# Performance work log

Hardware: AMD Instinct MI355X
Metric: run time of the kernel (lower is better)

Reference implementation:

```python
import jax, jax.numpy as jnp
import numpy as np
from math import sqrt

B, IN_C, OUT_C, H, W, WDIM, K = 16, 512, 512, 64, 64, 512, 3
EPS = 1e-8
LRELU_SLOPE = 0.2


def setup_inputs() -> dict:
    key = jax.random.key(0)
    ks = jax.random.split(key, 5)
    return {
        "x": jax.random.normal(ks[0], (B, IN_C, H, W), dtype=jnp.float32),
        "w": jax.random.normal(ks[1], (B, WDIM), dtype=jnp.float32),
        "noise": jax.random.normal(ks[2], (B, 1, H, W), dtype=jnp.float32),
        "linear_w": jax.random.normal(ks[3], (IN_C, WDIM), dtype=jnp.float32),
        "linear_b": jnp.ones((IN_C,), dtype=jnp.float32),
        "conv_w": jax.random.normal(ks[4], (OUT_C, IN_C, K, K), dtype=jnp.float32),
        "scale_noise": jnp.zeros((OUT_C,), dtype=jnp.float32),
        "bias": jnp.zeros((OUT_C,), dtype=jnp.float32),
    }


def reference(x, w, noise, linear_w, linear_b, conv_w, scale_noise, bias):
    # EqualizerStraights: equalized-lr linear, scale = 1/sqrt(w_dim)
    s = w @ (linear_w * (1.0 / sqrt(WDIM))).T + linear_b  # [b, in_c]
    # Weight_Demod: equalized conv weight, scale = 1/sqrt(in_c*k*k)
    base_w = conv_w * (1.0 / sqrt(IN_C * K * K))  # [out, in, k, k]
    weights = base_w[None] * s[:, None, :, None, None]  # [b, out, in, k, k]
    sigma_inv = jax.lax.rsqrt(
        jnp.sum(weights * weights, axis=(2, 3, 4), keepdims=True) + EPS)
    weights = weights * sigma_inv

    def conv1(xi, wi):  # xi [in,h,w], wi [out,in,k,k]
        return jax.lax.conv_general_dilated(
            xi[None], wi, window_strides=(1, 1), padding="SAME",
            dimension_numbers=("NCHW", "OIHW", "NCHW"))[0]

    y = jax.vmap(conv1)(x, weights)  # [b, out, h, w]
    y = y + scale_noise[None, :, None, None] * noise
    return jax.nn.leaky_relu(y + bias[None, :, None, None], negative_slope=LRELU_SLOPE)
```

## Files before the change

### kernel.cpp

```cpp
#include <hip/hip_runtime.h>
#include <hip/hip_bf16.h>
#include <stdint.h>

typedef __bf16 bf16_t;
typedef __bf16 bf16x8 __attribute__((ext_vector_type(8)));
typedef short short8 __attribute__((ext_vector_type(8)));
typedef float f32x4 __attribute__((ext_vector_type(4)));

#define RS512  0.044194173824159216f
#define RS4608 0.014731391274719739f

__global__ void k_style(const float* __restrict__ w, const float* __restrict__ lw,
                        const float* __restrict__ lb, float* __restrict__ s) {
  int b = blockIdx.y;
  int c = blockIdx.x * 256 + threadIdx.x;
  const float4* wr = (const float4*)(w + b * 512);
  const float4* lr = (const float4*)(lw + (size_t)c * 512);
  float acc = 0.f;
#pragma unroll 4
  for (int d = 0; d < 128; ++d) {
    float4 a = wr[d], q = lr[d];
    acc += a.x * q.x + a.y * q.y + a.z * q.z + a.w * q.w;
  }
  s[b * 512 + c] = acc * RS512 + lb[c];
}

__global__ void k_wprep(const float* __restrict__ cw, float* __restrict__ wsq,
                        bf16_t* __restrict__ bwf) {
  int idx = blockIdx.x * 256 + threadIdx.x;
  int o = idx >> 9, i = idx & 511;
  float v[9];
  float ss = 0.f;
#pragma unroll
  for (int t = 0; t < 9; ++t) {
    float x = cw[(size_t)idx * 9 + t] * RS4608;
    v[t] = x;
    ss += x * x;
  }
  wsq[idx] = ss;
  int lane = (o & 15) | (((i >> 3) & 3) << 4);
  int base_blk = (i >> 5) * 32 + (o >> 4);
#pragma unroll
  for (int t = 0; t < 9; ++t) {
    size_t e = ((size_t)(t * 512 + base_blk) << 9) + lane * 8 + (i & 7);
    bwf[e] = (bf16_t)v[t];
  }
}

__global__ void k_sigma(const float* __restrict__ s, const float* __restrict__ wsq,
                        float* __restrict__ sinv) {
  __shared__ float s2[512];
  int b = blockIdx.y;
  int o = blockIdx.x * 256 + threadIdx.x;
  for (int i = threadIdx.x; i < 512; i += 256) {
    float v = s[b * 512 + i];
    s2[i] = v * v;
  }
  __syncthreads();
  const float4* qr = (const float4*)(wsq + (size_t)o * 512);
  float acc = 0.f;
#pragma unroll 4
  for (int d = 0; d < 128; ++d) {
    float4 q = qr[d];
    acc += q.x * s2[4 * d] + q.y * s2[4 * d + 1] + q.z * s2[4 * d + 2] + q.w * s2[4 * d + 3];
  }
  sinv[b * 512 + o] = rsqrtf(acc + 1e-8f);
}

__global__ void k_xt(const float* __restrict__ x, const float* __restrict__ s,
                     bf16_t* __restrict__ xt) {
  int ic = blockIdx.x, h = blockIdx.y, b = blockIdx.z;
  __shared__ __align__(16) bf16_t tile[8192];
  int t = threadIdx.x;
  int wcol = t & 63;
  int g = t >> 6;
#pragma unroll
  for (int blk = 0; blk < 4; ++blk) {
    int grp = blk * 4 + g;
    bf16x8 vec;
#pragma unroll
    for (int k = 0; k < 8; ++k) {
      int i = ic * 128 + grp * 8 + k;
      float v = x[(((size_t)b * 512 + i) * 64 + h) * 64 + wcol] * s[b * 512 + i];
      vec[k] = (bf16_t)v;
    }
    int chunk = grp ^ (wcol & 15);
    *(bf16x8*)((char*)tile + wcol * 256 + chunk * 16) = vec;
  }
  __syncthreads();
#pragma unroll
  for (int j = 0; j < 4; ++j) {
    int flat = j * 256 + t;
    int wo = flat >> 4, ig8 = flat & 15;
    int chunk = ig8 ^ (wo & 15);
    bf16x8 v = *(bf16x8*)((char*)tile + wo * 256 + chunk * 16);
    int c32 = (ig8 >> 2);
    int slot = (ig8 & 3) ^ ((wo >> 1) & 3);
    *(bf16x8*)(xt + (((size_t)b * 64 + h) * 64 + wo) * 512 + ic * 128 + c32 * 32 + slot * 8) = v;
  }
}

#define AS1 __attribute__((address_space(1)))
#define AS3 __attribute__((address_space(3)))

__device__ __forceinline__ void gl16(const void* g, void* l) {
  __builtin_amdgcn_global_load_lds((const AS1 void*)g, (AS3 void*)l, 16, 0, 0);
}

#define VMCNT(n) asm volatile("s_waitcnt vmcnt(" #n ")" ::: "memory")

__global__ __launch_bounds__(256, 2) void k_conv(
    const bf16_t* __restrict__ xt, const bf16_t* __restrict__ bwf,
    const float* __restrict__ sinv, const float* __restrict__ noise,
    const float* __restrict__ snz, const float* __restrict__ bias,
    float* __restrict__ out) {
  __shared__ __align__(16) char lds[77824];

  const int t = threadIdx.x;
  const int rq = blockIdx.x;
  const int oy = blockIdx.y;
  const int b = blockIdx.z;
  const int h0 = rq * 4;
  const int lane = t & 63;
  const int wv = t >> 6;
  const int wm = wv >> 1;
  const int wn = wv & 1;

  const char* xg = (const char*)xt + (size_t)b * 4194304 + (t >> 2) * 1024 + (t & 3) * 16;
  const char* wg = (const char*)bwf + ((size_t)(oy * 8 + wv * 2) << 10) + (lane << 4);

  f32x4 acc[4][8] = {};

  const uint32_t woff = (uint32_t)((wm << 12) + (lane << 4));
  uint32_t pXcol[4][3];
#pragma unroll
  for (int j = 0; j < 4; ++j)
#pragma unroll
    for (int dk = 0; dk < 3; ++dk) {
      int icol = j * 16 + (lane & 15) + dk - 1;
      int ic2 = icol < 0 ? 0 : (icol > 63 ? 63 : icol);
      int slot = (lane >> 4) ^ ((ic2 >> 1) & 3);
      pXcol[j][dk] = (uint32_t)(24576 + wn * 8192 + ic2 * 64 + slot * 16);
    }
  const bool c0 = (lane & 15) == 0;
  const bool c15 = (lane & 15) == 15;

  auto stageXrow = [&](int c, int buf, int r) {
    int gr = h0 - 1 + r;
    if ((unsigned)gr < 64u) {
      gl16(xg + (size_t)gr * 65536 + c * 64, lds + 24576 + buf * 24576 + r * 4096 + (wv << 10));
    } else {
      gl16(xg + c * 64, lds + 73728 + (wv << 10));
    }
  };

  auto stageW = [&](int cc, int tt, int buf) {
    const char* s0 = wg + (size_t)(tt * 16 + cc) * 32768;
    char* d0 = lds + buf * 8192 + (wv << 11);
    gl16(s0, d0);
    gl16(s0 + 1024, d0 + 1024);
  };

  auto compute_tap = [&](int XB, int tap) {
    const int ky = tap / 3, kx = tap % 3;
    bf16x8 af[4];
#pragma unroll
    for (int mi = 0; mi < 4; ++mi)
      af[mi] = *(const bf16x8*)(lds + woff + (uint32_t)((tap % 3) * 8192 + mi * 1024));
    bf16x8 bfr[8];
#pragma unroll
    for (int ni = 0; ni < 8; ++ni) {
      short8 xv = *(const short8*)(lds + pXcol[ni & 3][kx] +
                                   (uint32_t)(XB * 24576 + ((ni >> 2) + ky) * 4096));
      if (kx == 0 && (ni & 3) == 0) xv = c0 ? (short8)0 : xv;
      if (kx == 2 && (ni & 3) == 3) xv = c15 ? (short8)0 : xv;
      bfr[ni] = __builtin_bit_cast(bf16x8, xv);
    }
    __builtin_amdgcn_s_setprio(1);
#pragma unroll
    for (int mi = 0; mi < 4; ++mi)
#pragma unroll
      for (int ni = 0; ni < 8; ++ni)
        acc[mi][ni] =
            __builtin_amdgcn_mfma_f32_16x16x32_bf16(af[mi], bfr[ni], acc[mi][ni], 0, 0, 0);
    __builtin_amdgcn_s_setprio(0);
  };

#define PHASE(c, tp, LAST, XB)                                                 \
  {                                                                            \
    if (!(LAST) && (tp) < 6) stageXrow((c) + 1, (XB) ^ 1, (tp));               \
    if (!(LAST) || (tp) <= 6) {                                                \
      if ((tp) + 2 <= 8) stageW((c), (tp) + 2, ((tp) + 2) % 3);                \
      else stageW((c) + 1, (tp) - 7, ((tp) + 2) % 3);                          \
    }                                                                          \
    if (LAST) {                                                                \
      if ((tp) <= 6) { VMCNT(4); }                                             \
      else if ((tp) == 7) { VMCNT(2); }                                        \
      else { VMCNT(0); }                                                       \
    } else {                                                                   \
      if ((tp) == 0 || (tp) == 6) { VMCNT(5); }                                \
      else if ((tp) <= 5) { VMCNT(6); }                                        \
      else { VMCNT(4); }                                                       \
    }                                                                          \
    __builtin_amdgcn_s_barrier();                                              \
    compute_tap((XB), (tp));                                                   \
  }

  if (h0 == 0) {
    *(f32x4*)(lds + 24576 + t * 16) = (f32x4)0.f;
    *(f32x4*)(lds + 49152 + t * 16) = (f32x4)0.f;
  }
  if (h0 == 60) {
    *(f32x4*)(lds + 24576 + 5 * 4096 + t * 16) = (f32x4)0.f;
    *(f32x4*)(lds + 49152 + 5 * 4096 + t * 16) = (f32x4)0.f;
  }
  asm volatile("s_waitcnt lgkmcnt(0)" ::: "memory");
#pragma unroll
  for (int r = 0; r < 6; ++r) stageXrow(0, 0, r);
  stageW(0, 0, 0);
  stageW(0, 1, 1);

#pragma unroll 1
  for (int ci = 0; ci < 7; ++ci) {
    const int ce = ci * 2;
#pragma unroll
    for (int tp = 0; tp < 9; ++tp) PHASE(ce, tp, 0, 0);
#pragma unroll
    for (int tp = 0; tp < 9; ++tp) PHASE(ce + 1, tp, 0, 1);
  }
#pragma unroll
  for (int tp = 0; tp < 9; ++tp) PHASE(14, tp, 0, 0);
#pragma unroll
  for (int tp = 0; tp < 9; ++tp) PHASE(15, tp, 1, 1);

  const float* sb = sinv + b * 512;
  const int og = oy * 128 + wm * 64 + ((lane >> 4) << 2);
  const int colb = lane & 15;
  float nzv[8];
#pragma unroll
  for (int ni = 0; ni < 8; ++ni) {
    int prow = h0 + wn * 2 + (ni >> 2);
    int col = (ni & 3) * 16 + colb;
    nzv[ni] = noise[(size_t)b * 4096 + prow * 64 + col];
  }
#pragma unroll
  for (int mi = 0; mi < 4; ++mi) {
#pragma unroll
    for (int r = 0; r < 4; ++r) {
      int o = og + mi * 16 + r;
      float sv = sb[o];
      float nw = snz[o];
      float bv = bias[o];
      float* obase = out + ((size_t)b * 512 + o) * 4096;
#pragma unroll
      for (int ni = 0; ni < 8; ++ni) {
        int prow = h0 + wn * 2 + (ni >> 2);
        int col = (ni & 3) * 16 + colb;
        float v = acc[mi][ni][r] * sv + nw * nzv[ni] + bv;
        obase[prow * 64 + col] = v > 0.f ? v : 0.2f * v;
      }
    }
  }
}

extern "C" void kernel_launch(void* const* d_in, const int* in_sizes, int n_in,
                              void* d_out, int out_size, void* d_ws, size_t ws_size,
                              hipStream_t stream) {
  const float* x     = (const float*)d_in[0];
  const float* w     = (const float*)d_in[1];
  const float* noise = (const float*)d_in[2];
  const float* lw    = (const float*)d_in[3];
  const float* lb    = (const float*)d_in[4];
  const float* cw    = (const float*)d_in[5];
  const float* snz   = (const float*)d_in[6];
  const float* bias  = (const float*)d_in[7];
  float* out = (float*)d_out;

  char* ws = (char*)d_ws;
  bf16_t* xt   = (bf16_t*)ws;
  bf16_t* bwf  = (bf16_t*)(ws + 67108864);
  float*  s    = (float*)(ws + 71827456);
  float*  sinv = (float*)(ws + 71860224);
  float*  wsq  = (float*)(ws + 71892992);

  k_style<<<dim3(2, 16), 256, 0, stream>>>(w, lw, lb, s);
  k_wprep<<<dim3(1024), 256, 0, stream>>>(cw, wsq, bwf);
  k_sigma<<<dim3(2, 16), 256, 0, stream>>>(s, wsq, sinv);
  k_xt<<<dim3(4, 64, 16), 256, 0, stream>>>(x, s, xt);
  k_conv<<<dim3(16, 4, 16), 256, 0, stream>>>(xt, bwf, sinv, noise, snz, bias, out);
}
```

Before: 299.8 us.

## Double conv block tile to 8 rows with 512 threads and ky-grouped weight staging

The conv kernel now uses 512-thread blocks, each covering 8 output rows instead of 4, which halves the grid. Weight tiles are staged in groups of three taps (one kernel row), and each barrier is followed by three MFMA taps instead of one. The goal is more reuse of each staged weight and fewer barriers per input-channel chunk. The cost is one block per CU with about 153KB of LDS, which leaves less latency hiding across blocks, plus a rewritten wait-count schedule that is easy to get wrong.

New measurement: 322.6 us. 7.6% more time.

```diff
diff --git a/kernel.cpp b/kernel.cpp
--- a/kernel.cpp
+++ b/kernel.cpp
@@ -109,30 +109,52 @@
 
 #define VMCNT(n) asm volatile("s_waitcnt vmcnt(" #n ")" ::: "memory")
 
-__global__ __launch_bounds__(256, 2) void k_conv(
+__global__ __launch_bounds__(512, 1) void k_conv(
     const bf16_t* __restrict__ xt, const bf16_t* __restrict__ bwf,
     const float* __restrict__ sinv, const float* __restrict__ noise,
     const float* __restrict__ snz, const float* __restrict__ bias,
     float* __restrict__ out) {
-  __shared__ __align__(16) char lds[77824];
+  __shared__ __align__(16) char lds[156672];
 
   const int t = threadIdx.x;
   const int rq = blockIdx.x;
-  const int oy = blockIdx.y;
+  const int OY = blockIdx.y;
   const int b = blockIdx.z;
-  const int h0 = rq * 4;
+  const int h0 = rq * 8;
   const int lane = t & 63;
   const int wv = t >> 6;
-  const int wm = wv >> 1;
-  const int wn = wv & 1;
-
-  const char* xg = (const char*)xt + (size_t)b * 4194304 + (t >> 2) * 1024 + (t & 3) * 16;
-  const char* wg = (const char*)bwf + ((size_t)(oy * 8 + wv * 2) << 10) + (lane << 4);
+  const int wm = wv & 1;
+  const int wn = wv >> 1;
+
+  const char* xtb = (const char*)xt + (size_t)b * 4194304;
+  const char* xg = xtb + (lane >> 2) * 1024 + (lane & 3) * 16;
+  const char* wg = (const char*)bwf + OY * 8192 + lane * 16;
 
   f32x4 acc[4][8] = {};
 
-  const uint32_t woff = (uint32_t)((wm << 12) + (lane << 4));
-  uint32_t pXcol[4][3];
+  uint32_t xsrcOff[5], xdstOff[5], xadd[5];
+#pragma unroll
+  for (int j = 0; j < 5; ++j) {
+    int fl = wv * 5 + j, row = fl >> 2, q = fl & 3;
+    int gr = h0 - 1 + row;
+    int v = ((unsigned)gr < 64u) ? 1 : 0;
+    xsrcOff[j] = __builtin_amdgcn_readfirstlane(v ? (uint32_t)(gr * 65536 + q * 16384) : 0u);
+    xdstOff[j] = __builtin_amdgcn_readfirstlane(
+        v ? (uint32_t)(73728 + row * 4096 + q * 1024) : 155648u);
+    xadd[j] = __builtin_amdgcn_readfirstlane(v ? 40960u : 0u);
+  }
+  uint32_t wsrcOff[3], wdstOff[3];
+#pragma unroll
+  for (int k = 0; k < 3; ++k) {
+    int fl = wv * 3 + k, tp = fl >> 3, fr = fl & 7;
+    wsrcOff[k] = __builtin_amdgcn_readfirstlane((uint32_t)(tp * 524288 + fr * 1024));
+    wdstOff[k] = __builtin_amdgcn_readfirstlane((uint32_t)(tp * 8192 + fr * 1024));
+  }
+
+  uint32_t woffG[3];
+#pragma unroll
+  for (int g = 0; g < 3; ++g) woffG[g] = (uint32_t)(g * 24576 + wm * 4096 + lane * 16);
+  uint32_t pX[4][3];
 #pragma unroll
   for (int j = 0; j < 4; ++j)
 #pragma unroll
@@ -140,108 +162,103 @@
       int icol = j * 16 + (lane & 15) + dk - 1;
       int ic2 = icol < 0 ? 0 : (icol > 63 ? 63 : icol);
       int slot = (lane >> 4) ^ ((ic2 >> 1) & 3);
-      pXcol[j][dk] = (uint32_t)(24576 + wn * 8192 + ic2 * 64 + slot * 16);
+      pX[j][dk] = (uint32_t)(73728 + wn * 8192 + ic2 * 64 + slot * 16);
     }
   const bool c0 = (lane & 15) == 0;
   const bool c15 = (lane & 15) == 15;
 
-  auto stageXrow = [&](int c, int buf, int r) {
-    int gr = h0 - 1 + r;
-    if ((unsigned)gr < 64u) {
-      gl16(xg + (size_t)gr * 65536 + c * 64, lds + 24576 + buf * 24576 + r * 4096 + (wv << 10));
-    } else {
-      gl16(xg + c * 64, lds + 73728 + (wv << 10));
+  auto stX = [&](int j, uint32_t co, int bufflag) {
+    gl16(xg + xsrcOff[j] + co, lds + xdstOff[j] + (bufflag ? xadd[j] : 0u));
+  };
+  auto stW = [&](int k, uint32_t gco, int buf) {
+    gl16(wg + wsrcOff[k] + gco, lds + wdstOff[k] + buf * 24576);
+  };
+
+  auto comp = [&](int XB, int G) {
+#pragma unroll
+    for (int kx = 0; kx < 3; ++kx) {
+      bf16x8 af[4];
+#pragma unroll
+      for (int mi = 0; mi < 4; ++mi)
+        af[mi] = *(const bf16x8*)(lds + woffG[G] + (uint32_t)(kx * 8192 + mi * 1024));
+      bf16x8 bfr[8];
+#pragma unroll
+      for (int ni = 0; ni < 8; ++ni) {
+        short8 xv = *(const short8*)(lds + pX[ni & 3][kx] +
+                                     (uint32_t)(XB * 40960 + ((ni >> 2) + G) * 4096));
+        if (kx == 0 && (ni & 3) == 0) xv = c0 ? (short8)0 : xv;
+        if (kx == 2 && (ni & 3) == 3) xv = c15 ? (short8)0 : xv;
+        bfr[ni] = __builtin_bit_cast(bf16x8, xv);
+      }
+      __builtin_amdgcn_s_setprio(1);
+#pragma unroll
+      for (int mi = 0; mi < 4; ++mi)
+#pragma unroll
+        for (int ni = 0; ni < 8; ++ni)
+          acc[mi][ni] =
+              __builtin_amdgcn_mfma_f32_16x16x32_bf16(af[mi], bfr[ni], acc[mi][ni], 0, 0, 0);
+      __builtin_amdgcn_s_setprio(0);
     }
   };
 
-  auto stageW = [&](int cc, int tt, int buf) {
-    const char* s0 = wg + (size_t)(tt * 16 + cc) * 32768;
-    char* d0 = lds + buf * 8192 + (wv << 11);
-    gl16(s0, d0);
-    gl16(s0 + 1024, d0 + 1024);
-  };
-
-  auto compute_tap = [&](int XB, int tap) {
-    const int ky = tap / 3, kx = tap % 3;
-    bf16x8 af[4];
-#pragma unroll
-    for (int mi = 0; mi < 4; ++mi)
-      af[mi] = *(const bf16x8*)(lds + woff + (uint32_t)((tap % 3) * 8192 + mi * 1024));
-    bf16x8 bfr[8];
-#pragma unroll
-    for (int ni = 0; ni < 8; ++ni) {
-      short8 xv = *(const short8*)(lds + pXcol[ni & 3][kx] +
-                                   (uint32_t)(XB * 24576 + ((ni >> 2) + ky) * 4096));
-      if (kx == 0 && (ni & 3) == 0) xv = c0 ? (short8)0 : xv;
-      if (kx == 2 && (ni & 3) == 3) xv = c15 ? (short8)0 : xv;
-      bfr[ni] = __builtin_bit_cast(bf16x8, xv);
-    }
-    __builtin_amdgcn_s_setprio(1);
-#pragma unroll
-    for (int mi = 0; mi < 4; ++mi)
-#pragma unroll
-      for (int ni = 0; ni < 8; ++ni)
-        acc[mi][ni] =
-            __builtin_amdgcn_mfma_f32_16x16x32_bf16(af[mi], bfr[ni], acc[mi][ni], 0, 0, 0);
-    __builtin_amdgcn_s_setprio(0);
-  };
-
-#define PHASE(c, tp, LAST, XB)                                                 \
+#define GBODY(XB, CXO, CW, LAST)                                               \
   {                                                                            \
-    if (!(LAST) && (tp) < 6) stageXrow((c) + 1, (XB) ^ 1, (tp));               \
-    if (!(LAST) || (tp) <= 6) {                                                \
-      if ((tp) + 2 <= 8) stageW((c), (tp) + 2, ((tp) + 2) % 3);                \
-      else stageW((c) + 1, (tp) - 7, ((tp) + 2) % 3);                          \
+    stW(0, 1572864u + (CW), 1); stW(1, 1572864u + (CW), 1);                    \
+    stW(2, 1572864u + (CW), 1);                                                \
+    VMCNT(3);                                                                  \
+    __builtin_amdgcn_s_barrier();                                              \
+    comp((XB), 0);                                                             \
+    if (!(LAST)) {                                                             \
+      stX(0, (CXO), (XB) ^ 1); stX(1, (CXO), (XB) ^ 1); stX(2, (CXO), (XB) ^ 1);\
     }                                                                          \
-    if (LAST) {                                                                \
-      if ((tp) <= 6) { VMCNT(4); }                                             \
-      else if ((tp) == 7) { VMCNT(2); }                                        \
-      else { VMCNT(0); }                                                       \
+    stW(0, 3145728u + (CW), 2); stW(1, 3145728u + (CW), 2);                    \
+    stW(2, 3145728u + (CW), 2);                                                \
+    if (LAST) { VMCNT(3); } else { VMCNT(6); }                                 \
+    __builtin_amdgcn_s_barrier();                                              \
+    comp((XB), 1);                                                             \
+    if (!(LAST)) {                                                             \
+      stX(3, (CXO), (XB) ^ 1); stX(4, (CXO), (XB) ^ 1);                        \
+      stW(0, (CW) + 32768u, 0); stW(1, (CW) + 32768u, 0);                      \
+      stW(2, (CW) + 32768u, 0);                                                \
+      VMCNT(5);                                                                \
     } else {                                                                   \
-      if ((tp) == 0 || (tp) == 6) { VMCNT(5); }                                \
-      else if ((tp) <= 5) { VMCNT(6); }                                        \
-      else { VMCNT(4); }                                                       \
+      VMCNT(0);                                                                \
     }                                                                          \
     __builtin_amdgcn_s_barrier();                                              \
-    compute_tap((XB), (tp));                                                   \
-  }
-
-  if (h0 == 0) {
-    *(f32x4*)(lds + 24576 + t * 16) = (f32x4)0.f;
-    *(f32x4*)(lds + 49152 + t * 16) = (f32x4)0.f;
-  }
-  if (h0 == 60) {
-    *(f32x4*)(lds + 24576 + 5 * 4096 + t * 16) = (f32x4)0.f;
-    *(f32x4*)(lds + 49152 + 5 * 4096 + t * 16) = (f32x4)0.f;
-  }
+    comp((XB), 2);                                                             \
+  }
+
+  if (rq == 0)
+    *(f32x4*)(lds + 73728 + (t >> 8) * 40960 + (t & 255) * 16) = (f32x4)0.f;
+  if (rq == 7)
+    *(f32x4*)(lds + 73728 + (t >> 8) * 40960 + 9 * 4096 + (t & 255) * 16) = (f32x4)0.f;
   asm volatile("s_waitcnt lgkmcnt(0)" ::: "memory");
 #pragma unroll
-  for (int r = 0; r < 6; ++r) stageXrow(0, 0, r);
-  stageW(0, 0, 0);
-  stageW(0, 1, 1);
-
+  for (int j = 0; j < 5; ++j) stX(j, 0u, 0);
+  stW(0, 0u, 0); stW(1, 0u, 0); stW(2, 0u, 0);
+  VMCNT(0);
+  __builtin_amdgcn_s_barrier();
+
+  uint32_t cw = 0, cxo = 64;
 #pragma unroll 1
   for (int ci = 0; ci < 7; ++ci) {
-    const int ce = ci * 2;
-#pragma unroll
-    for (int tp = 0; tp < 9; ++tp) PHASE(ce, tp, 0, 0);
-#pragma unroll
-    for (int tp = 0; tp < 9; ++tp) PHASE(ce + 1, tp, 0, 1);
-  }
-#pragma unroll
-  for (int tp = 0; tp < 9; ++tp) PHASE(14, tp, 0, 0);
-#pragma unroll
-  for (int tp = 0; tp < 9; ++tp) PHASE(15, tp, 1, 1);
+    GBODY(0, cxo, cw, 0);
+    cw += 32768u; cxo += 64u;
+    GBODY(1, cxo, cw, 0);
+    cw += 32768u; cxo += 64u;
+  }
+  GBODY(0, cxo, cw, 0);
+  cw += 32768u;
+  GBODY(1, 0u, cw, 1);
 
   const float* sb = sinv + b * 512;
-  const int og = oy * 128 + wm * 64 + ((lane >> 4) << 2);
+  const int og = OY * 128 + wm * 64 + ((lane >> 4) << 2);
   const int colb = lane & 15;
   float nzv[8];
 #pragma unroll
   for (int ni = 0; ni < 8; ++ni) {
     int prow = h0 + wn * 2 + (ni >> 2);
-    int col = (ni & 3) * 16 + colb;
-    nzv[ni] = noise[(size_t)b * 4096 + prow * 64 + col];
+    nzv[ni] = noise[(size_t)b * 4096 + prow * 64 + (ni & 3) * 16 + colb];
   }
 #pragma unroll
   for (int mi = 0; mi < 4; ++mi) {
@@ -287,5 +304,5 @@
   k_wprep<<<dim3(1024), 256, 0, stream>>>(cw, wsq, bwf);
   k_sigma<<<dim3(2, 16), 256, 0, stream>>>(s, wsq, sinv);
   k_xt<<<dim3(4, 64, 16), 256, 0, stream>>>(x, s, xt);
-  k_conv<<<dim3(16, 4, 16), 256, 0, stream>>>(xt, bwf, sinv, noise, snz, bias, out);
-}
+  k_conv<<<dim3(8, 4, 16), 512, 0, stream>>>(xt, bwf, sinv, noise, snz, bias, out);
+}
```

## Restructure conv pipeline to two-tap stages with fewer barriers and zero-row buffer

Applied to the files above, without the earlier changes.

The conv main loop now processes two taps per barrier stage instead of one. It uses double-buffered pairs of weight slices (16KB each) and issues X-row loads for the next channel chunk interleaved with compute. Out-of-range halo rows are now loaded from a global zero buffer initialized by k_wprep, replacing the in-LDS zeroing and shared dummy slot. This halves barrier count and simplifies waitcnt accounting, at the cost of more LDS (80KB) and a deeper dependency on the new schedule being race-free.

New measurement: 299.7 us. No clear change (-0.0%).

```diff
diff --git a/kernel.cpp b/kernel.cpp
--- a/kernel.cpp
+++ b/kernel.cpp
@@ -26,7 +26,8 @@
 }
 
 __global__ void k_wprep(const float* __restrict__ cw, float* __restrict__ wsq,
-                        bf16_t* __restrict__ bwf) {
+                        bf16_t* __restrict__ bwf, f32x4* __restrict__ zb) {
+  if (blockIdx.x == 0) zb[threadIdx.x] = (f32x4)0.f;
   int idx = blockIdx.x * 256 + threadIdx.x;
   int o = idx >> 9, i = idx & 511;
   float v[9];
@@ -108,17 +109,18 @@
 }
 
 #define VMCNT(n) asm volatile("s_waitcnt vmcnt(" #n ")" ::: "memory")
+#define BAR __builtin_amdgcn_s_barrier()
 
 __global__ __launch_bounds__(256, 2) void k_conv(
     const bf16_t* __restrict__ xt, const bf16_t* __restrict__ bwf,
     const float* __restrict__ sinv, const float* __restrict__ noise,
     const float* __restrict__ snz, const float* __restrict__ bias,
-    float* __restrict__ out) {
-  __shared__ __align__(16) char lds[77824];
+    const char* __restrict__ zb, float* __restrict__ out) {
+  __shared__ __align__(16) char lds[81920];
 
   const int t = threadIdx.x;
   const int rq = blockIdx.x;
-  const int oy = blockIdx.y;
+  const int OY = blockIdx.y;
   const int b = blockIdx.z;
   const int h0 = rq * 4;
   const int lane = t & 63;
@@ -127,12 +129,13 @@
   const int wn = wv & 1;
 
   const char* xg = (const char*)xt + (size_t)b * 4194304 + (t >> 2) * 1024 + (t & 3) * 16;
-  const char* wg = (const char*)bwf + ((size_t)(oy * 8 + wv * 2) << 10) + (lane << 4);
+  const char* wgp = (const char*)bwf + OY * 8192 + wv * 2048 + lane * 16;
+  const char* zgv = zb + t * 16;
 
   f32x4 acc[4][8] = {};
 
   const uint32_t woff = (uint32_t)((wm << 12) + (lane << 4));
-  uint32_t pXcol[4][3];
+  uint32_t pX[4][3];
 #pragma unroll
   for (int j = 0; j < 4; ++j)
 #pragma unroll
@@ -140,37 +143,33 @@
       int icol = j * 16 + (lane & 15) + dk - 1;
       int ic2 = icol < 0 ? 0 : (icol > 63 ? 63 : icol);
       int slot = (lane >> 4) ^ ((ic2 >> 1) & 3);
-      pXcol[j][dk] = (uint32_t)(24576 + wn * 8192 + ic2 * 64 + slot * 16);
+      pX[j][dk] = (uint32_t)(32768 + wn * 8192 + ic2 * 64 + slot * 16);
     }
   const bool c0 = (lane & 15) == 0;
   const bool c15 = (lane & 15) == 15;
 
-  auto stageXrow = [&](int c, int buf, int r) {
+  auto stW = [&](uint32_t srcoff, uint32_t dst) {
+    const char* s0 = wgp + srcoff;
+    gl16(s0, lds + dst + (wv << 11));
+    gl16(s0 + 1024, lds + dst + (wv << 11) + 1024);
+  };
+  auto stX = [&](int r, uint32_t cxoff, int xb) {
     int gr = h0 - 1 + r;
-    if ((unsigned)gr < 64u) {
-      gl16(xg + (size_t)gr * 65536 + c * 64, lds + 24576 + buf * 24576 + r * 4096 + (wv << 10));
-    } else {
-      gl16(xg + c * 64, lds + 73728 + (wv << 10));
-    }
+    char* d = lds + 32768 + xb * 24576 + r * 4096 + (wv << 10);
+    if ((unsigned)gr < 64u) gl16(xg + (size_t)gr * 65536 + cxoff, d);
+    else gl16(zgv, d);
   };
 
-  auto stageW = [&](int cc, int tt, int buf) {
-    const char* s0 = wg + (size_t)(tt * 16 + cc) * 32768;
-    char* d0 = lds + buf * 8192 + (wv << 11);
-    gl16(s0, d0);
-    gl16(s0 + 1024, d0 + 1024);
-  };
-
-  auto compute_tap = [&](int XB, int tap) {
+  auto CT = [&](int XB, int tap, uint32_t WS) {
     const int ky = tap / 3, kx = tap % 3;
     bf16x8 af[4];
 #pragma unroll
     for (int mi = 0; mi < 4; ++mi)
-      af[mi] = *(const bf16x8*)(lds + woff + (uint32_t)((tap % 3) * 8192 + mi * 1024));
+      af[mi] = *(const bf16x8*)(lds + (woff + WS) + (uint32_t)(mi * 1024));
     bf16x8 bfr[8];
 #pragma unroll
     for (int ni = 0; ni < 8; ++ni) {
-      short8 xv = *(const short8*)(lds + pXcol[ni & 3][kx] +
+      short8 xv = *(const short8*)(lds + pX[ni & 3][kx] +
                                    (uint32_t)(XB * 24576 + ((ni >> 2) + ky) * 4096));
       if (kx == 0 && (ni & 3) == 0) xv = c0 ? (short8)0 : xv;
       if (kx == 2 && (ni & 3) == 3) xv = c15 ? (short8)0 : xv;
@@ -186,62 +185,75 @@
     __builtin_amdgcn_s_setprio(0);
   };
 
-#define PHASE(c, tp, LAST, XB)                                                 \
+#define UNIT(CWB, CXB, WA, WB, LAST)                                           \
   {                                                                            \
-    if (!(LAST) && (tp) < 6) stageXrow((c) + 1, (XB) ^ 1, (tp));               \
-    if (!(LAST) || (tp) <= 6) {                                                \
-      if ((tp) + 2 <= 8) stageW((c), (tp) + 2, ((tp) + 2) % 3);                \
-      else stageW((c) + 1, (tp) - 7, ((tp) + 2) % 3);                          \
+    stW((CWB) + 2u * 524288u, (WB)); stW((CWB) + 3u * 524288u, (WB) + 8192u);  \
+    stX(0, (CXB), 1); stX(1, (CXB), 1);                                        \
+    CT(0, 0, (WA)); CT(0, 1, (WA) + 8192u);                                    \
+    VMCNT(2); BAR;                                                             \
+    stW((CWB) + 4u * 524288u, (WA)); stW((CWB) + 5u * 524288u, (WA) + 8192u);  \
+    stX(2, (CXB), 1); stX(3, (CXB), 1);                                        \
+    CT(0, 2, (WB)); CT(0, 3, (WB) + 8192u);                                    \
+    VMCNT(2); BAR;                                                             \
+    stW((CWB) + 6u * 524288u, (WB)); stW((CWB) + 7u * 524288u, (WB) + 8192u);  \
+    stX(4, (CXB), 1); stX(5, (CXB), 1);                                        \
+    CT(0, 4, (WA)); CT(0, 5, (WA) + 8192u);                                    \
+    VMCNT(2); BAR;                                                             \
+    stW((CWB) + 8u * 524288u, (WA)); stW((CWB) + 32768u, (WA) + 8192u);        \
+    CT(0, 6, (WB)); CT(0, 7, (WB) + 8192u);                                    \
+    VMCNT(0); BAR;                                                             \
+    stW((CWB) + 32768u + 1u * 524288u, (WB));                                  \
+    stW((CWB) + 32768u + 2u * 524288u, (WB) + 8192u);                          \
+    CT(0, 8, (WA)); CT(1, 0, (WA) + 8192u);                                    \
+    VMCNT(0); BAR;                                                             \
+    stW((CWB) + 32768u + 3u * 524288u, (WA));                                  \
+    stW((CWB) + 32768u + 4u * 524288u, (WA) + 8192u);                          \
+    if (!(LAST)) { stX(0, (CXB) + 64u, 0); stX(1, (CXB) + 64u, 0); }           \
+    CT(1, 1, (WB)); CT(1, 2, (WB) + 8192u);                                    \
+    if (LAST) { VMCNT(0); } else { VMCNT(2); }                                 \
+    BAR;                                                                       \
+    stW((CWB) + 32768u + 5u * 524288u, (WB));                                  \
+    stW((CWB) + 32768u + 6u * 524288u, (WB) + 8192u);                          \
+    if (!(LAST)) { stX(2, (CXB) + 64u, 0); stX(3, (CXB) + 64u, 0); }           \
+    CT(1, 3, (WA)); CT(1, 4, (WA) + 8192u);                                    \
+    if (LAST) { VMCNT(0); } else { VMCNT(2); }                                 \
+    BAR;                                                                       \
+    stW((CWB) + 32768u + 7u * 524288u, (WA));                                  \
+    stW((CWB) + 32768u + 8u * 524288u, (WA) + 8192u);                          \
+    if (!(LAST)) { stX(4, (CXB) + 64u, 0); stX(5, (CXB) + 64u, 0); }           \
+    CT(1, 5, (WB)); CT(1, 6, (WB) + 8192u);                                    \
+    if (LAST) { VMCNT(0); } else { VMCNT(2); }                                 \
+    BAR;                                                                       \
+    if (!(LAST)) {                                                             \
+      stW((CWB) + 65536u, (WB)); stW((CWB) + 65536u + 524288u, (WB) + 8192u);  \
     }                                                                          \
-    if (LAST) {                                                                \
-      if ((tp) <= 6) { VMCNT(4); }                                             \
-      else if ((tp) == 7) { VMCNT(2); }                                        \
-      else { VMCNT(0); }                                                       \
-    } else {                                                                   \
-      if ((tp) == 0 || (tp) == 6) { VMCNT(5); }                                \
-      else if ((tp) <= 5) { VMCNT(6); }                                        \
-      else { VMCNT(4); }                                                       \
-    }                                                                          \
-    __builtin_amdgcn_s_barrier();                                              \
-    compute_tap((XB), (tp));                                                   \
-  }
-
-  if (h0 == 0) {
-    *(f32x4*)(lds + 24576 + t * 16) = (f32x4)0.f;
-    *(f32x4*)(lds + 49152 + t * 16) = (f32x4)0.f;
-  }
-  if (h0 == 60) {
-    *(f32x4*)(lds + 24576 + 5 * 4096 + t * 16) = (f32x4)0.f;
-    *(f32x4*)(lds + 49152 + 5 * 4096 + t * 16) = (f32x4)0.f;
-  }
-  asm volatile("s_waitcnt lgkmcnt(0)" ::: "memory");
-#pragma unroll
-  for (int r = 0; r < 6; ++r) stageXrow(0, 0, r);
-  stageW(0, 0, 0);
-  stageW(0, 1, 1);
-
+    CT(1, 7, (WA)); CT(1, 8, (WA) + 8192u);                                    \
+    if (!(LAST)) { VMCNT(0); BAR; }                                            \
+  }
+
+#pragma unroll
+  for (int r = 0; r < 6; ++r) stX(r, 0u, 0);
+  stW(0u, 0u); stW(524288u, 8192u);
+  VMCNT(0); BAR;
+
+  uint32_t cwb = 0, cxb = 64;
 #pragma unroll 1
-  for (int ci = 0; ci < 7; ++ci) {
-    const int ce = ci * 2;
-#pragma unroll
-    for (int tp = 0; tp < 9; ++tp) PHASE(ce, tp, 0, 0);
-#pragma unroll
-    for (int tp = 0; tp < 9; ++tp) PHASE(ce + 1, tp, 0, 1);
-  }
-#pragma unroll
-  for (int tp = 0; tp < 9; ++tp) PHASE(14, tp, 0, 0);
-#pragma unroll
-  for (int tp = 0; tp < 9; ++tp) PHASE(15, tp, 1, 1);
+  for (int k = 0; k < 7; ++k) {
+    const uint32_t wA = (uint32_t)(k & 1) << 14;
+    const uint32_t wB = wA ^ 16384u;
+    UNIT(cwb, cxb, wA, wB, 0);
+    cwb += 65536u; cxb += 128u;
+  }
+  UNIT(cwb, cxb, 16384u, 0u, 1);
 
   const float* sb = sinv + b * 512;
-  const int og = oy * 128 + wm * 64 + ((lane >> 4) << 2);
+  const int og = OY * 128 + wm * 64 + ((lane >> 4) << 2);
   const int colb = lane & 15;
   float nzv[8];
 #pragma unroll
   for (int ni = 0; ni < 8; ++ni) {
     int prow = h0 + wn * 2 + (ni >> 2);
-    int col = (ni & 3) * 16 + colb;
-    nzv[ni] = noise[(size_t)b * 4096 + prow * 64 + col];
+    nzv[ni] = noise[(size_t)b * 4096 + prow * 64 + (ni & 3) * 16 + colb];
   }
 #pragma unroll
   for (int mi = 0; mi < 4; ++mi) {
@@ -282,10 +294,11 @@
   float*  s    = (float*)(ws + 71827456);
   float*  sinv = (float*)(ws + 71860224);
   float*  wsq  = (float*)(ws + 71892992);
+  char*   zbuf = ws + 72941568;
 
   k_style<<<dim3(2, 16), 256, 0, stream>>>(w, lw, lb, s);
-  k_wprep<<<dim3(1024), 256, 0, stream>>>(cw, wsq, bwf);
+  k_wprep<<<dim3(1024), 256, 0, stream>>>(cw, wsq, bwf, (f32x4*)zbuf);
   k_sigma<<<dim3(2, 16), 256, 0, stream>>>(s, wsq, sinv);
   k_xt<<<dim3(4, 64, 16), 256, 0, stream>>>(x, s, xt);
-  k_conv<<<dim3(16, 4, 16), 256, 0, stream>>>(xt, bwf, sinv, noise, snz, bias, out);
-}
+  k_conv<<<dim3(16, 4, 16), 256, 0, stream>>>(xt, bwf, sinv, noise, snz, bias, zbuf, out);
+}
```
